# Optimization experiments

Measured on AMD Instinct MI355X. Metric: run time of the kernel, lower is better.

## Reference

```python
import jax, jax.numpy as jnp
import numpy as np

B, C, H, W = 2, 256, 64, 64
HEADS, DIM_HEAD = 8, 64
INNER = HEADS * DIM_HEAD


def setup_inputs() -> dict:
    key = jax.random.key(0)
    k1, k2, k3, k4 = jax.random.split(key, 4)
    x = jax.random.normal(k1, (B, C, H, W), dtype=jnp.float32)
    # 1x1 conv weights stored as [out_ch, in_ch]
    w_qkv = jax.random.normal(k2, (3 * INNER, C), dtype=jnp.float32) * (1.0 / np.sqrt(C))
    w_out = jax.random.normal(k3, (C, INNER), dtype=jnp.float32) * (1.0 / np.sqrt(INNER))
    b_out = jax.random.normal(k4, (C,), dtype=jnp.float32) * 0.01
    return {"x": x, "w_qkv": w_qkv, "w_out": w_out, "b_out": b_out}


def reference(x, w_qkv, w_out, b_out):
    b, c, h, w = x.shape
    n = h * w
    # 1x1 conv == channel matmul
    qkv = jnp.einsum('oc,bchw->bohw', w_qkv, x)  # [B, 3*inner, H, W]
    qkv = qkv.reshape(b, 3, HEADS, DIM_HEAD, n)
    qkv = jnp.transpose(qkv, (1, 0, 2, 4, 3))    # [3, B, heads, N, dim_head]
    q, k, v = qkv[0], qkv[1], qkv[2]
    scale = 1.0 / (DIM_HEAD ** 0.5)
    dots = jnp.einsum('bhnd,bhmd->bhnm', q, k) * scale  # [B, heads, N, N]
    attn = jax.nn.softmax(dots, axis=-1)
    out = jnp.einsum('bhnm,bhmd->bhnd', attn, v)        # [B, heads, N, dim_head]
    out = jnp.transpose(out, (0, 1, 3, 2)).reshape(b, INNER, h, w)
    return jnp.einsum('ci,bihw->bchw', w_out, out) + b_out[None, :, None, None]
```

## Files before the change

kernel.cpp:

```cpp
#include <hip/hip_runtime.h>
#include <hip/hip_bf16.h>

typedef unsigned short u16;
typedef __attribute__((ext_vector_type(8))) short bf16x8;
typedef __attribute__((ext_vector_type(4))) float f32x4;
typedef __attribute__((ext_vector_type(8))) unsigned short u16x8;
typedef __attribute__((ext_vector_type(4))) unsigned short u16x4;

#define N_POS 4096
#define HEADS 8
#define DHEAD 64
#define CIN   256
#define INNER 512
#define NSPLIT 2
#define JCHUNK (N_POS / NSPLIT)

__device__ __forceinline__ u16 f2bf(float f) {
    union { float f; unsigned int u; } v; v.f = f;
    unsigned int u = v.u + 0x7FFFu + ((v.u >> 16) & 1u);
    return (u16)(u >> 16);
}

__device__ __forceinline__ unsigned int pkbf2(float lo, float hi) {
    union { __hip_bfloat162 b; unsigned int u; } cv;
    cv.b = __float22bfloat162_rn(make_float2(lo, hi));
    return cv.u;
}

__global__ __launch_bounds__(256) void k0_prep(const float* __restrict__ x,
                                               const float* __restrict__ w_qkv,
                                               const float* __restrict__ w_out,
                                               u16* __restrict__ xT,
                                               u16* __restrict__ wq,
                                               u16* __restrict__ wo) {
    int bid = blockIdx.x;
    int t   = threadIdx.x;
    if (bid < 256) {
        int b = bid >> 7, rest = bid & 127;
        int n  = (rest & 15) * 256 + t;
        int c0 = (rest >> 4) * 32;
        const float* xp = x + (size_t)b * CIN * N_POS + n;
        u16* op = xT + ((size_t)(b * N_POS + n)) * CIN + c0;
        for (int g = 0; g < 4; ++g) {
            u16x8 v;
            for (int j = 0; j < 8; ++j)
                v[j] = f2bf(xp[(size_t)(c0 + g * 8 + j) * N_POS]);
            *(u16x8*)(op + g * 8) = v;
        }
    } else if (bid < 448) {
        size_t idx = (size_t)(bid - 256) * 2048 + t * 8;
        u16x8 v;
        for (int j = 0; j < 8; ++j) v[j] = f2bf(w_qkv[idx + j]);
        *(u16x8*)(wq + idx) = v;
    } else {
        size_t idx = (size_t)(bid - 448) * 2048 + t * 8;
        u16x8 v;
        for (int j = 0; j < 8; ++j) v[j] = f2bf(w_out[idx + j]);
        *(u16x8*)(wo + idx) = v;
    }
}

__global__ __launch_bounds__(256, 4) void k1_qkv(const u16* __restrict__ wq,
                                                 const u16* __restrict__ xT,
                                                 u16* __restrict__ q_ws,
                                                 u16* __restrict__ k_ws,
                                                 u16* __restrict__ vt_ws) {
    __shared__ u16 Alds[64 * 40];
    __shared__ u16 Blds[128 * 40];
    int tid = threadIdx.x;
    int n0  = blockIdx.x * 128;
    int by  = blockIdx.y;
    int b   = blockIdx.z;
    int o0  = by * 64;
    int sel = by >> 3;
    int h   = by & 7;
    int wv = tid >> 6, l = tid & 63, quad = l >> 4, l15 = l & 15;
    int srow = tid >> 2, sseg = tid & 3;
    int brow = tid >> 1, bseg = tid & 1;

    f32x4 acc[8] = {};
    for (int c0 = 0; c0 < CIN; c0 += 32) {
        *(u16x8*)&Alds[srow * 40 + sseg * 8] =
            *(const u16x8*)(wq + (size_t)(o0 + srow) * CIN + c0 + sseg * 8);
        const u16* xp = xT + ((size_t)(b * N_POS + n0 + brow)) * CIN + c0 + bseg * 16;
        *(u16x8*)&Blds[brow * 40 + bseg * 16]     = *(const u16x8*)xp;
        *(u16x8*)&Blds[brow * 40 + bseg * 16 + 8] = *(const u16x8*)(xp + 8);
        __syncthreads();
        bf16x8 af = *(const bf16x8*)&Alds[(wv * 16 + l15) * 40 + quad * 8];
        for (int nt = 0; nt < 8; ++nt) {
            bf16x8 bfrag = *(const bf16x8*)&Blds[(nt * 16 + l15) * 40 + quad * 8];
            acc[nt] = __builtin_amdgcn_mfma_f32_16x16x32_bf16(af, bfrag, acc[nt], 0, 0, 0);
        }
        __syncthreads();
    }
    const float QSCALE = 0.125f * 1.44269504088896f;
    float sc = (sel == 0) ? QSCALE : 1.0f;
    int dbase = wv * 16 + quad * 4;
    for (int nt = 0; nt < 8; ++nt) {
        int n = n0 + nt * 16 + l15;
        if (sel < 2) {
            u16* base = (sel == 0) ? q_ws : k_ws;
            u16x4 pk;
            for (int r = 0; r < 4; ++r) pk[r] = f2bf(acc[nt][r] * sc);
            *(u16x4*)&base[((size_t)((b * HEADS + h) * N_POS + n)) * DHEAD + dbase] = pk;
        } else {
            for (int r = 0; r < 4; ++r)
                vt_ws[((size_t)((b * HEADS + h) * DHEAD + dbase + r)) * N_POS + n] =
                    f2bf(acc[nt][r]);
        }
    }
}

__global__ __launch_bounds__(512, 4) void k2_attn(const u16* __restrict__ q_ws,
                                                  const u16* __restrict__ k_ws,
                                                  const u16* __restrict__ vt_ws,
                                                  float* __restrict__ op_ws,
                                                  float* __restrict__ lw_ws) {
    __shared__ u16 Klds[64 * 72];
    __shared__ u16 Vlds[64 * 72];
    int tid = threadIdx.x;
    int q0  = blockIdx.x * 256;
    int bh  = blockIdx.y;
    int half = blockIdx.z;
    int jbase = half * JCHUNK;
    int wv = tid >> 6, l = tid & 63, quad = l >> 4, l15 = l & 15;
    int srow = tid >> 3, sseg = tid & 7;
    int srowp = (srow & 0x23) | ((srow & 4) << 2) | ((srow & 0x18) >> 1);

    const u16* qp = q_ws + ((size_t)(bh * N_POS + q0 + wv * 32 + l15)) * DHEAD + quad * 8;
    bf16x8 bq[2][2];
    for (int it = 0; it < 2; ++it) {
        bq[it][0] = *(const bf16x8*)(qp + (size_t)it * 16 * DHEAD);
        bq[it][1] = *(const bf16x8*)(qp + (size_t)it * 16 * DHEAD + 32);
    }

    f32x4 Oacc[2][4] = {};
    float lsum[2] = {0.f, 0.f};

    const u16* kp = k_ws + ((size_t)(bh * N_POS + srow)) * DHEAD + sseg * 8;
    const u16* vp = vt_ws + ((size_t)(bh * DHEAD + srow)) * N_POS + sseg * 8;

    u16x8 pf0 = *(const u16x8*)(kp + (size_t)jbase * DHEAD);
    u16x8 pf1 = *(const u16x8*)(vp + jbase);

    for (int j0 = jbase; j0 < jbase + JCHUNK; j0 += 64) {
        *(u16x8*)&Klds[srowp * 72 + sseg * 8] = pf0;
        *(u16x8*)&Vlds[srow * 72 + sseg * 8]  = pf1;
        __syncthreads();

        if (j0 + 64 < jbase + JCHUNK) {
            pf0 = *(const u16x8*)(kp + (size_t)(j0 + 64) * DHEAD);
            pf1 = *(const u16x8*)(vp + j0 + 64);
        }

        unsigned int pkw[2][2][4];
        for (int p = 0; p < 2; ++p)
            for (int a = 0; a < 2; ++a) {
                const u16* kb = &Klds[((2 * p + a) * 16 + l15) * 72 + quad * 8];
                bf16x8 kf0 = *(const bf16x8*)kb;
                bf16x8 kf1 = *(const bf16x8*)(kb + 32);
                f32x4 z[2];
                __builtin_amdgcn_s_setprio(1);
                for (int it = 0; it < 2; ++it) {
                    f32x4 t = {};
                    t = __builtin_amdgcn_mfma_f32_16x16x32_bf16(kf0, bq[it][0], t, 0, 0, 0);
                    t = __builtin_amdgcn_mfma_f32_16x16x32_bf16(kf1, bq[it][1], t, 0, 0, 0);
                    z[it] = t;
                }
                __builtin_amdgcn_s_setprio(0);
                for (int it = 0; it < 2; ++it) {
                    float e0 = __builtin_amdgcn_exp2f(z[it][0]);
                    float e1 = __builtin_amdgcn_exp2f(z[it][1]);
                    float e2 = __builtin_amdgcn_exp2f(z[it][2]);
                    float e3 = __builtin_amdgcn_exp2f(z[it][3]);
                    lsum[it] += (e0 + e1) + (e2 + e3);
                    pkw[it][p][2 * a]     = pkbf2(e0, e1);
                    pkw[it][p][2 * a + 1] = pkbf2(e2, e3);
                }
            }

        __builtin_amdgcn_s_setprio(1);
        for (int dt = 0; dt < 4; ++dt)
            for (int p = 0; p < 2; ++p) {
                bf16x8 vf = *(const bf16x8*)&Vlds[(dt * 16 + l15) * 72 + p * 32 + quad * 8];
                for (int it = 0; it < 2; ++it) {
                    union { unsigned int u[4]; bf16x8 v; } cv;
                    cv.u[0] = pkw[it][p][0]; cv.u[1] = pkw[it][p][1];
                    cv.u[2] = pkw[it][p][2]; cv.u[3] = pkw[it][p][3];
                    Oacc[it][dt] = __builtin_amdgcn_mfma_f32_16x16x32_bf16(vf, cv.v, Oacc[it][dt], 0, 0, 0);
                }
            }
        __builtin_amdgcn_s_setprio(0);
        __syncthreads();
    }

    int b = bh >> 3, h = bh & 7;
    float* opb = op_ws + (size_t)half * 2 * N_POS * INNER;
    float* lwb = lw_ws + (size_t)half * 2 * HEADS * N_POS;
    for (int it = 0; it < 2; ++it) {
        float ls = lsum[it];
        ls += __shfl_xor(ls, 16);
        ls += __shfl_xor(ls, 32);
        int n = q0 + wv * 32 + it * 16 + l15;
        if (quad == 0) lwb[(size_t)bh * N_POS + n] = ls;
        float* dst = opb + ((size_t)(b * N_POS + n)) * INNER + h * DHEAD;
        for (int dt = 0; dt < 4; ++dt)
            *(f32x4*)&dst[dt * 16 + quad * 4] = Oacc[it][dt];
    }
}

__global__ __launch_bounds__(256) void k3_out(const u16* __restrict__ wo,
                                              const float* __restrict__ b_out,
                                              const float* __restrict__ op_ws,
                                              const float* __restrict__ lw_ws,
                                              float* __restrict__ out) {
    __shared__ u16 Alds[64 * 40];
    __shared__ u16 Blds[64 * 40];
    int tid = threadIdx.x;
    int n0 = blockIdx.x * 64;
    int c0 = blockIdx.y * 64;
    int b  = blockIdx.z;
    int wv = tid >> 6, l = tid & 63, quad = l >> 4, l15 = l & 15;
    int srow = tid >> 2, sseg = tid & 3;

    f32x4 acc[4] = {};
    for (int i0 = 0; i0 < INNER; i0 += 32) {
        *(u16x8*)&Alds[srow * 40 + sseg * 8] =
            *(const u16x8*)(wo + (size_t)(c0 + srow) * INNER + i0 + sseg * 8);
        {
            int i = i0 + sseg * 8;
            int h = i >> 6;
            int n = n0 + srow;
            size_t lidx = ((size_t)(b * HEADS + h)) * N_POS + n;
            float ls = lw_ws[lidx] + lw_ws[(size_t)2 * HEADS * N_POS + lidx];
            float inv = 1.0f / ls;
            const float* p0 = op_ws + ((size_t)(b * N_POS + n)) * INNER + i;
            const float* p1 = p0 + (size_t)2 * N_POS * INNER;
            f32x4 a0 = *(const f32x4*)p0, a1 = *(const f32x4*)(p0 + 4);
            f32x4 b0 = *(const f32x4*)p1, b1 = *(const f32x4*)(p1 + 4);
            u16x8 v;
            for (int k = 0; k < 4; ++k) v[k]     = f2bf((a0[k] + b0[k]) * inv);
            for (int k = 0; k < 4; ++k) v[4 + k] = f2bf((a1[k] + b1[k]) * inv);
            *(u16x8*)&Blds[srow * 40 + sseg * 8] = v;
        }
        __syncthreads();
        bf16x8 af = *(const bf16x8*)&Alds[(wv * 16 + l15) * 40 + quad * 8];
        for (int nt = 0; nt < 4; ++nt) {
            bf16x8 bfrag = *(const bf16x8*)&Blds[(nt * 16 + l15) * 40 + quad * 8];
            acc[nt] = __builtin_amdgcn_mfma_f32_16x16x32_bf16(af, bfrag, acc[nt], 0, 0, 0);
        }
        __syncthreads();
    }
    for (int r = 0; r < 4; ++r) {
        int c = c0 + wv * 16 + quad * 4 + r;
        float bias = b_out[c];
        for (int nt = 0; nt < 4; ++nt) {
            int n = n0 + nt * 16 + l15;
            out[((size_t)(b * CIN + c)) * N_POS + n] = acc[nt][r] + bias;
        }
    }
}

extern "C" void kernel_launch(void* const* d_in, const int* in_sizes, int n_in,
                              void* d_out, int out_size, void* d_ws, size_t ws_size,
                              hipStream_t stream) {
    const float* x     = (const float*)d_in[0];
    const float* w_qkv = (const float*)d_in[1];
    const float* w_out = (const float*)d_in[2];
    const float* b_out = (const float*)d_in[3];
    float* out = (float*)d_out;

    u16* ws    = (u16*)d_ws;
    u16* xT    = ws;
    u16* q_ws  = xT   + (size_t)2 * N_POS * CIN;
    u16* k_ws  = q_ws + (size_t)2 * HEADS * N_POS * DHEAD;
    u16* vt_ws = k_ws + (size_t)2 * HEADS * N_POS * DHEAD;
    u16* wq_bf = vt_ws + (size_t)2 * HEADS * N_POS * DHEAD;
    u16* wo_bf = wq_bf + (size_t)3 * INNER * CIN;
    float* op_ws = (float*)(wo_bf + (size_t)CIN * INNER);
    float* lw_ws = op_ws + (size_t)NSPLIT * 2 * N_POS * INNER;

    hipLaunchKernelGGL(k0_prep, dim3(512), dim3(256), 0, stream,
                       x, w_qkv, w_out, xT, wq_bf, wo_bf);
    hipLaunchKernelGGL(k1_qkv, dim3(32, 24, 2), dim3(256), 0, stream,
                       wq_bf, xT, q_ws, k_ws, vt_ws);
    hipLaunchKernelGGL(k2_attn, dim3(16, 16, NSPLIT), dim3(512), 0, stream,
                       q_ws, k_ws, vt_ws, op_ws, lw_ws);
    hipLaunchKernelGGL(k3_out, dim3(64, 4, 2), dim3(256), 0, stream,
                       wo_bf, b_out, op_ws, lw_ws, out);
}
```

Baseline: 182.1 us.

## Drop attention key split, normalize in-kernel, and retile output projection over all channels

The attention kernel no longer splits the key range in two. Each block now loops over all 4096 keys, normalizes by the row sum itself, and writes bf16 output directly. This removes the fp32 partial-output and row-sum workspaces and the combine step in the output projection. The output projection kernel is retiled so each block covers all 256 output channels for 32 positions and reads bf16 activations. This cuts global traffic, but it halves the attention grid to 256 blocks, which may leave compute units idle and lengthen the serial key loop per block.

```diff
diff --git a/kernel.cpp b/kernel.cpp
--- a/kernel.cpp
+++ b/kernel.cpp
@@ -12,8 +12,6 @@
 #define DHEAD 64
 #define CIN   256
 #define INNER 512
-#define NSPLIT 2
-#define JCHUNK (N_POS / NSPLIT)
 
 __device__ __forceinline__ u16 f2bf(float f) {
     union { float f; unsigned int u; } v; v.f = f;
@@ -114,15 +112,12 @@
 __global__ __launch_bounds__(512, 4) void k2_attn(const u16* __restrict__ q_ws,
                                                   const u16* __restrict__ k_ws,
                                                   const u16* __restrict__ vt_ws,
-                                                  float* __restrict__ op_ws,
-                                                  float* __restrict__ lw_ws) {
+                                                  u16* __restrict__ obf) {
     __shared__ u16 Klds[64 * 72];
     __shared__ u16 Vlds[64 * 72];
     int tid = threadIdx.x;
     int q0  = blockIdx.x * 256;
     int bh  = blockIdx.y;
-    int half = blockIdx.z;
-    int jbase = half * JCHUNK;
     int wv = tid >> 6, l = tid & 63, quad = l >> 4, l15 = l & 15;
     int srow = tid >> 3, sseg = tid & 7;
     int srowp = (srow & 0x23) | ((srow & 4) << 2) | ((srow & 0x18) >> 1);
@@ -140,15 +135,15 @@
     const u16* kp = k_ws + ((size_t)(bh * N_POS + srow)) * DHEAD + sseg * 8;
     const u16* vp = vt_ws + ((size_t)(bh * DHEAD + srow)) * N_POS + sseg * 8;
 
-    u16x8 pf0 = *(const u16x8*)(kp + (size_t)jbase * DHEAD);
-    u16x8 pf1 = *(const u16x8*)(vp + jbase);
-
-    for (int j0 = jbase; j0 < jbase + JCHUNK; j0 += 64) {
+    u16x8 pf0 = *(const u16x8*)kp;
+    u16x8 pf1 = *(const u16x8*)vp;
+
+    for (int j0 = 0; j0 < N_POS; j0 += 64) {
         *(u16x8*)&Klds[srowp * 72 + sseg * 8] = pf0;
         *(u16x8*)&Vlds[srow * 72 + sseg * 8]  = pf1;
         __syncthreads();
 
-        if (j0 + 64 < jbase + JCHUNK) {
+        if (j0 + 64 < N_POS) {
             pf0 = *(const u16x8*)(kp + (size_t)(j0 + 64) * DHEAD);
             pf1 = *(const u16x8*)(vp + j0 + 64);
         }
@@ -195,70 +190,63 @@
     }
 
     int b = bh >> 3, h = bh & 7;
-    float* opb = op_ws + (size_t)half * 2 * N_POS * INNER;
-    float* lwb = lw_ws + (size_t)half * 2 * HEADS * N_POS;
     for (int it = 0; it < 2; ++it) {
         float ls = lsum[it];
         ls += __shfl_xor(ls, 16);
         ls += __shfl_xor(ls, 32);
+        float inv = 1.0f / ls;
         int n = q0 + wv * 32 + it * 16 + l15;
-        if (quad == 0) lwb[(size_t)bh * N_POS + n] = ls;
-        float* dst = opb + ((size_t)(b * N_POS + n)) * INNER + h * DHEAD;
-        for (int dt = 0; dt < 4; ++dt)
-            *(f32x4*)&dst[dt * 16 + quad * 4] = Oacc[it][dt];
+        u16* dst = obf + ((size_t)(b * N_POS + n)) * INNER + h * DHEAD;
+        for (int dt = 0; dt < 4; ++dt) {
+            u16x4 pk;
+            for (int r = 0; r < 4; ++r) pk[r] = f2bf(Oacc[it][dt][r] * inv);
+            *(u16x4*)&dst[dt * 16 + quad * 4] = pk;
+        }
     }
 }
 
 __global__ __launch_bounds__(256) void k3_out(const u16* __restrict__ wo,
                                               const float* __restrict__ b_out,
-                                              const float* __restrict__ op_ws,
-                                              const float* __restrict__ lw_ws,
+                                              const u16* __restrict__ obf,
                                               float* __restrict__ out) {
-    __shared__ u16 Alds[64 * 40];
-    __shared__ u16 Blds[64 * 40];
+    __shared__ u16 Alds[256 * 40];
+    __shared__ u16 Blds[32 * 40];
     int tid = threadIdx.x;
-    int n0 = blockIdx.x * 64;
-    int c0 = blockIdx.y * 64;
-    int b  = blockIdx.z;
+    int n0 = blockIdx.x * 32;
+    int b  = blockIdx.y;
     int wv = tid >> 6, l = tid & 63, quad = l >> 4, l15 = l & 15;
-    int srow = tid >> 2, sseg = tid & 3;
-
-    f32x4 acc[4] = {};
+
+    f32x4 acc[4][2] = {};
     for (int i0 = 0; i0 < INNER; i0 += 32) {
-        *(u16x8*)&Alds[srow * 40 + sseg * 8] =
-            *(const u16x8*)(wo + (size_t)(c0 + srow) * INNER + i0 + sseg * 8);
-        {
-            int i = i0 + sseg * 8;
-            int h = i >> 6;
-            int n = n0 + srow;
-            size_t lidx = ((size_t)(b * HEADS + h)) * N_POS + n;
-            float ls = lw_ws[lidx] + lw_ws[(size_t)2 * HEADS * N_POS + lidx];
-            float inv = 1.0f / ls;
-            const float* p0 = op_ws + ((size_t)(b * N_POS + n)) * INNER + i;
-            const float* p1 = p0 + (size_t)2 * N_POS * INNER;
-            f32x4 a0 = *(const f32x4*)p0, a1 = *(const f32x4*)(p0 + 4);
-            f32x4 b0 = *(const f32x4*)p1, b1 = *(const f32x4*)(p1 + 4);
-            u16x8 v;
-            for (int k = 0; k < 4; ++k) v[k]     = f2bf((a0[k] + b0[k]) * inv);
-            for (int k = 0; k < 4; ++k) v[4 + k] = f2bf((a1[k] + b1[k]) * inv);
-            *(u16x8*)&Blds[srow * 40 + sseg * 8] = v;
-        }
-        __syncthreads();
-        bf16x8 af = *(const bf16x8*)&Alds[(wv * 16 + l15) * 40 + quad * 8];
-        for (int nt = 0; nt < 4; ++nt) {
-            bf16x8 bfrag = *(const bf16x8*)&Blds[(nt * 16 + l15) * 40 + quad * 8];
-            acc[nt] = __builtin_amdgcn_mfma_f32_16x16x32_bf16(af, bfrag, acc[nt], 0, 0, 0);
-        }
-        __syncthreads();
-    }
-    for (int r = 0; r < 4; ++r) {
-        int c = c0 + wv * 16 + quad * 4 + r;
-        float bias = b_out[c];
-        for (int nt = 0; nt < 4; ++nt) {
-            int n = n0 + nt * 16 + l15;
-            out[((size_t)(b * CIN + c)) * N_POS + n] = acc[nt][r] + bias;
-        }
-    }
+        for (int rep = 0; rep < 4; ++rep) {
+            int row = rep * 64 + (tid >> 2), seg = tid & 3;
+            *(u16x8*)&Alds[row * 40 + seg * 8] =
+                *(const u16x8*)(wo + (size_t)row * INNER + i0 + seg * 8);
+        }
+        if (tid < 128) {
+            int srow = tid >> 2, sseg = tid & 3;
+            *(u16x8*)&Blds[srow * 40 + sseg * 8] =
+                *(const u16x8*)(obf + ((size_t)(b * N_POS + n0 + srow)) * INNER + i0 + sseg * 8);
+        }
+        __syncthreads();
+        for (int ac = 0; ac < 4; ++ac) {
+            bf16x8 af = *(const bf16x8*)&Alds[(wv * 64 + ac * 16 + l15) * 40 + quad * 8];
+            for (int nt = 0; nt < 2; ++nt) {
+                bf16x8 bfrag = *(const bf16x8*)&Blds[(nt * 16 + l15) * 40 + quad * 8];
+                acc[ac][nt] = __builtin_amdgcn_mfma_f32_16x16x32_bf16(af, bfrag, acc[ac][nt], 0, 0, 0);
+            }
+        }
+        __syncthreads();
+    }
+    for (int ac = 0; ac < 4; ++ac)
+        for (int r = 0; r < 4; ++r) {
+            int c = wv * 64 + ac * 16 + quad * 4 + r;
+            float bias = b_out[c];
+            for (int nt = 0; nt < 2; ++nt) {
+                int n = n0 + nt * 16 + l15;
+                out[((size_t)(b * CIN + c)) * N_POS + n] = acc[ac][nt][r] + bias;
+            }
+        }
 }
 
 extern "C" void kernel_launch(void* const* d_in, const int* in_sizes, int n_in,
@@ -277,15 +265,14 @@
     u16* vt_ws = k_ws + (size_t)2 * HEADS * N_POS * DHEAD;
     u16* wq_bf = vt_ws + (size_t)2 * HEADS * N_POS * DHEAD;
     u16* wo_bf = wq_bf + (size_t)3 * INNER * CIN;
-    float* op_ws = (float*)(wo_bf + (size_t)CIN * INNER);
-    float* lw_ws = op_ws + (size_t)NSPLIT * 2 * N_POS * INNER;
+    u16* obf   = wo_bf + (size_t)CIN * INNER;
 
     hipLaunchKernelGGL(k0_prep, dim3(512), dim3(256), 0, stream,
                        x, w_qkv, w_out, xT, wq_bf, wo_bf);
     hipLaunchKernelGGL(k1_qkv, dim3(32, 24, 2), dim3(256), 0, stream,
                        wq_bf, xT, q_ws, k_ws, vt_ws);
-    hipLaunchKernelGGL(k2_attn, dim3(16, 16, NSPLIT), dim3(512), 0, stream,
-                       q_ws, k_ws, vt_ws, op_ws, lw_ws);
-    hipLaunchKernelGGL(k3_out, dim3(64, 4, 2), dim3(256), 0, stream,
-                       wo_bf, b_out, op_ws, lw_ws, out);
-}
+    hipLaunchKernelGGL(k2_attn, dim3(16, 16), dim3(512), 0, stream,
+                       q_ws, k_ws, vt_ws, obf);
+    hipLaunchKernelGGL(k3_out, dim3(128, 2), dim3(256), 0, stream,
+                       wo_bf, b_out, obf, out);
+}
```

Measured after the change: 189.0 us. 1.04x slower.
